# Optimization experiments

Measured on AMD Instinct MI355X. Metric: run time of the kernel, lower is better.

## Reference

```python
import jax, jax.numpy as jnp
import numpy as np

LN_EPS = 1e-5
WKV_EPS = 1e-8
NEG_INF = -1e38


def _layernorm(x, g, b):
    m = jnp.mean(x, axis=-1, keepdims=True)
    v = jnp.mean(jnp.square(x - m), axis=-1, keepdims=True)
    return (x - m) * jax.lax.rsqrt(v + LN_EPS) * g + b


def _wkv(w, u, k, v):
    """RWKV WKV linear recurrence with log-sum-exp stabilized state.
    w,u: (C,); k,v: (B,T,C). Returns y (B,T,C), new_state (B,C,2)."""
    B, T, C = k.shape
    aa0 = jnp.zeros((B, C), k.dtype)
    bb0 = jnp.full((B, C), NEG_INF, k.dtype)

    def step(carry, kv_t):
        aa, bb = carry
        kk, vv = kv_t  # (B,C) each
        ww = u + kk
        p = jnp.maximum(bb, ww)
        e1 = jnp.exp(bb - p)
        e2 = jnp.exp(ww - p)
        y_t = (e1 * aa + e2 * vv) / (e1 + e2 + WKV_EPS)
        ww = w + bb
        p = jnp.maximum(ww, kk)
        e1 = jnp.exp(ww - p)
        e2 = jnp.exp(kk - p)
        aa = e1 * aa + e2 * vv
        bb = p + jnp.log(e1 + e2 + WKV_EPS)
        return (aa, bb), y_t

    (aa, bb), ys = jax.lax.scan(step, (aa0, bb0),
                                (jnp.swapaxes(k, 0, 1), jnp.swapaxes(v, 0, 1)))
    y = jnp.swapaxes(ys, 0, 1)  # (B,T,C)
    new_state = jnp.stack([aa, bb], axis=-1)  # (B,C,2)
    return y, new_state


def setup_inputs() -> dict:
    key = jax.random.key(0)
    ks = jax.random.split(key, 12)
    B, T, C = 8, 2048, 1024
    scale = 0.02
    return {
        "x": jax.random.normal(ks[0], (B, T, C), jnp.float32),
        "time_decay": jax.random.uniform(ks[1], (C,), jnp.float32, -1.0, 1.0),
        "time_first": jax.random.uniform(ks[2], (C,), jnp.float32, -1.0, 1.0),
        "W_tm": jax.random.normal(ks[3], (C, 3 * C), jnp.float32) * scale,
        "g1": jnp.ones((C,), jnp.float32),
        "b1": jnp.zeros((C,), jnp.float32),
        "tmk": jax.random.uniform(ks[4], (1, 1, C), jnp.float32),
        "tmv": jax.random.uniform(ks[5], (1, 1, C), jnp.float32),
        "tmr": jax.random.uniform(ks[6], (1, 1, C), jnp.float32),
        "W_cm": jax.random.normal(ks[7], (C, 4 * C), jnp.float32) * scale,
        "W_cp": jax.random.normal(ks[8], (4 * C, C), jnp.float32) * scale,
        "g2": jnp.ones((C,), jnp.float32),
        "b2": jnp.zeros((C,), jnp.float32),
        "cmk": jax.random.uniform(ks[9], (1, 1, C), jnp.float32),
        "cmr": jax.random.uniform(ks[10], (1, 1, C), jnp.float32),
    }


def reference(x, time_decay, time_first, W_tm, g1, b1, tmk, tmv, tmr,
              W_cm, W_cp, g2, b2, cmk, cmr):
    # ---- time mixing ----
    x_prev = jnp.concatenate([x[:, :1], x[:, :-1]], axis=1)  # shift (state=None)
    kvr = _layernorm(x, g1, b1) @ W_tm  # (B,T,3C)
    k, v, r = jnp.split(kvr, 3, axis=-1)
    k = k * tmk + x_prev * (1.0 - tmk)
    v = v * tmv + x_prev * (1.0 - tmv)
    r = jax.nn.sigmoid(r * tmr + x_prev * (1.0 - tmr))
    y, new_state = _wkv(time_decay, time_first, k, v)
    x = x + r * y
    # ---- channel mixing ----
    xp = jnp.concatenate([x[:, -1:], x[:, :-1]], axis=1)  # as in source
    xn = _layernorm(x, g2, b2)
    kk = xn @ W_cm  # (B,T,4C) hidden
    cmk4 = jnp.tile(cmk, (1, 1, 4))
    xp4 = jnp.tile(xp, (1, 1, 4))
    kk = kk * cmk4 + xp4 * (1.0 - cmk4)
    rr = jax.nn.sigmoid(xn * cmr + xp * (1.0 - cmr))
    vv = jnp.square(jax.nn.relu(kk)) @ W_cp  # (B,T,C)
    x = x + rr * vv
    return x, new_state
```

## Files before the change

kernel.cpp:

```cpp
#include <hip/hip_runtime.h>


#define Bb 8
#define T 2048
#define C 1024
#define M (Bb*T)
#define LCH 32
#define NCH 64
#define NCI (Bb*NCH)
#define WKV_THREADS (NCI*C)

typedef unsigned short u16;
typedef unsigned int u32;
typedef __bf16 bf16x8 __attribute__((ext_vector_type(8)));
typedef float f32x4 __attribute__((ext_vector_type(4)));
typedef u16 u16x4 __attribute__((ext_vector_type(4)));

__device__ __forceinline__ u16 f2bf(float f) {
    u32 u = __float_as_uint(f);
    u32 r = u + 0x7FFFu + ((u >> 16) & 1u);
    return (u16)(r >> 16);
}
__device__ __forceinline__ float bf2f(u16 s) {
    return __uint_as_float(((u32)s) << 16);
}
__device__ __forceinline__ float sigmoidf_(float z) {
    return 1.0f / (1.0f + __expf(-z));
}
__device__ __forceinline__ void load_lds16(const void* g, void* l) {
    __builtin_amdgcn_global_load_lds(
        (const __attribute__((address_space(1))) void*)g,
        (__attribute__((address_space(3))) void*)l, 16, 0, 0);
}

__global__ __launch_bounds__(256) void transpose_cast_kernel(
    const float* __restrict__ W, u16* __restrict__ Wt, int K, int N)
{
    __shared__ float tile[32][33];
    const int bk = blockIdx.x * 32, bn = blockIdx.y * 32;
    const int tx = threadIdx.x, ty = threadIdx.y;
    #pragma unroll
    for (int i = 0; i < 32; i += 8)
        tile[ty + i][tx] = W[(size_t)(bk + ty + i) * N + bn + tx];
    __syncthreads();
    #pragma unroll
    for (int i = 0; i < 32; i += 8)
        Wt[(size_t)(bn + ty + i) * K + bk + tx] = f2bf(tile[tx][ty + i]);
}

__device__ __forceinline__ void gemm_mainloop(
    const u16* __restrict__ A, const int lda,
    const u16* __restrict__ Bt, const int ldb, const int K,
    const int m0, const int n0, u16* Alds, u16* Blds, f32x4 acc[4][4])
{
    const int tid  = threadIdx.x;
    const int wave = tid >> 6, lane = tid & 63;
    const int q = lane >> 4, m16 = lane & 15;
    const int wr = (wave >> 1) << 6, wc = (wave & 1) << 6;

    const f32x4 zero4 = {0.f, 0.f, 0.f, 0.f};
    #pragma unroll
    for (int i = 0; i < 4; i++)
        #pragma unroll
        for (int j = 0; j < 4; j++) acc[i][j] = zero4;

    const int sr = tid >> 3;
    const int sc = (((tid & 7) ^ (sr & 7)) * 8);
    const u16* ag = &A[(size_t)(m0 + sr) * lda + sc];
    const u16* bg = &Bt[(size_t)(n0 + sr) * ldb + sc];
    u16* al = &Alds[tid * 8];
    u16* bl = &Blds[tid * 8];

    const int xh = (m16 & 7);

    for (int k0 = 0; k0 < K; k0 += 64) {
        #pragma unroll
        for (int t = 0; t < 4; ++t) {
            load_lds16(ag + (size_t)(t * 32) * lda + k0, al + t * 2048);
            load_lds16(bg + (size_t)(t * 32) * ldb + k0, bl + t * 2048);
        }
        __syncthreads();
        #pragma unroll
        for (int s = 0; s < 2; ++s) {
            const int ch = ((s * 4 + q) ^ xh) * 8;
            bf16x8 a[4], b[4];
            #pragma unroll
            for (int i = 0; i < 4; i++)
                a[i] = *(const bf16x8*)&Alds[(wr + i * 16 + m16) * 64 + ch];
            #pragma unroll
            for (int j = 0; j < 4; j++)
                b[j] = *(const bf16x8*)&Blds[(wc + j * 16 + m16) * 64 + ch];
            #pragma unroll
            for (int i = 0; i < 4; i++)
                #pragma unroll
                for (int j = 0; j < 4; j++)
                    acc[i][j] = __builtin_amdgcn_mfma_f32_16x16x32_bf16(a[i], b[j], acc[i][j], 0, 0, 0);
        }
        __syncthreads();
    }
}

__global__ __launch_bounds__(256) void ln1_kernel(
    const float* __restrict__ x, const float* __restrict__ g, const float* __restrict__ b,
    u16* __restrict__ xn)
{
    const int row = blockIdx.x, tid = threadIdx.x;
    const size_t base = (size_t)row * C;
    const int c = tid * 4;
    float4 v = *(const float4*)&x[base + c];
    float s  = v.x + v.y + v.z + v.w;
    float s2 = v.x*v.x + v.y*v.y + v.z*v.z + v.w*v.w;
    #pragma unroll
    for (int off = 32; off >= 1; off >>= 1) { s += __shfl_xor(s, off); s2 += __shfl_xor(s2, off); }
    __shared__ float red[8];
    const int wave = tid >> 6, lane = tid & 63;
    if (lane == 0) { red[wave] = s; red[4 + wave] = s2; }
    __syncthreads();
    const float sum  = red[0] + red[1] + red[2] + red[3];
    const float sums = red[4] + red[5] + red[6] + red[7];
    const float mean = sum * (1.0f / C);
    const float var  = sums * (1.0f / C) - mean * mean;
    const float rstd = rsqrtf(var + 1e-5f);
    float4 gv = *(const float4*)&g[c];
    float4 bv = *(const float4*)&b[c];
    u16x4 o;
    o.x = f2bf((v.x - mean) * rstd * gv.x + bv.x);
    o.y = f2bf((v.y - mean) * rstd * gv.y + bv.y);
    o.z = f2bf((v.z - mean) * rstd * gv.z + bv.z);
    o.w = f2bf((v.w - mean) * rstd * gv.w + bv.w);
    *(u16x4*)&xn[base + c] = o;
}

__global__ __launch_bounds__(256) void gemm1_kernel(
    const u16* __restrict__ xn, const u16* __restrict__ wt,
    const float* __restrict__ x,
    const float* __restrict__ tmk, const float* __restrict__ tmv, const float* __restrict__ tmr,
    u16* __restrict__ kvbuf, u16* __restrict__ rbuf)
{
    __shared__ __align__(16) u16 Alds[128 * 64];
    __shared__ __align__(16) u16 Blds[128 * 64];
    f32x4 acc[4][4];
    const int m0 = blockIdx.x * 128, n0 = blockIdx.y * 128;
    gemm_mainloop(xn, C, wt, C, C, m0, n0, Alds, Blds, acc);

    const int tid = threadIdx.x, wave = tid >> 6, lane = tid & 63;
    const int q = lane >> 4, m16 = lane & 15;
    const int wr = (wave >> 1) << 6, wc = (wave & 1) << 6;
    const int grp = n0 >> 10;
    const int cbase = (n0 & 1023) + wc;
    #pragma unroll
    for (int i = 0; i < 4; i++) {
        #pragma unroll
        for (int rg = 0; rg < 4; rg++) {
            const int row = m0 + wr + i * 16 + q * 4 + rg;
            const int t = row & (T - 1);
            const size_t rowp = (size_t)(t ? row - 1 : row) * C;
            #pragma unroll
            for (int j = 0; j < 4; j++) {
                const int cc = cbase + j * 16 + m16;
                const float val = acc[i][j][rg];
                const float xp = x[rowp + cc];
                if (grp == 0) {
                    const float f = tmk[cc];
                    kvbuf[(size_t)row * 2048 + 2 * cc] = f2bf(val * f + xp * (1.0f - f));
                } else if (grp == 1) {
                    const float f = tmv[cc];
                    kvbuf[(size_t)row * 2048 + 2 * cc + 1] = f2bf(val * f + xp * (1.0f - f));
                } else {
                    const float f = tmr[cc];
                    rbuf[(size_t)row * C + cc] = f2bf(sigmoidf_(val * f + xp * (1.0f - f)));
                }
            }
        }
    }
}

__global__ __launch_bounds__(256) void wkv_k1(
    const u32* __restrict__ kvp, const float* __restrict__ wdec, float* __restrict__ bc)
{
    const int tid = blockIdx.x * 256 + threadIdx.x;
    const int c = tid & (C - 1), ci = tid >> 10;
    const float w = wdec[c];
    const size_t L = ((size_t)(ci >> 6) * T + (size_t)(ci & (NCH - 1)) * LCH) * C + c;
    float bb = -1e38f;
    #pragma unroll 4
    for (int t = 0; t < LCH; ++t) {
        const float k = bf2f((u16)(kvp[L + (size_t)t * C] & 0xffffu));
        const float ww = w + bb;
        const float p = fmaxf(ww, k);
        const float e1 = __expf(ww - p), e2 = __expf(k - p);
        bb = p + __logf(e1 + e2 + 1e-8f);
    }
    bc[tid] = bb;
}

__global__ __launch_bounds__(256) void wkv_p1(
    const float* __restrict__ bc, const float* __restrict__ wdec, float* __restrict__ bbin)
{
    const int gid = blockIdx.x * 256 + threadIdx.x;
    const int c = gid & (C - 1), b = gid >> 10;
    const float Lw = (float)LCH * wdec[c];
    float bb = -1e38f;
    #pragma unroll 8
    for (int j = 0; j < NCH; ++j) {
        const int idx = (b * NCH + j) * C + c;
        bbin[idx] = bb;
        const float a = Lw + bb;
        const float bcv = bc[idx];
        const float m = fmaxf(a, bcv);
        bb = m + __logf(__expf(a - m) + __expf(bcv - m));
    }
}

__global__ __launch_bounds__(256) void wkv_k2a(
    const u32* __restrict__ kvp, const float* __restrict__ wdec,
    const float* __restrict__ bbin, float* __restrict__ logS, float* __restrict__ Rr)
{
    const int tid = blockIdx.x * 256 + threadIdx.x;
    const int c = tid & (C - 1), ci = tid >> 10;
    const float w = wdec[c];
    const size_t L = ((size_t)(ci >> 6) * T + (size_t)(ci & (NCH - 1)) * LCH) * C + c;
    float bb = bbin[tid], ls = 0.0f, R = 0.0f;
    #pragma unroll 4
    for (int t = 0; t < LCH; ++t) {
        const u32 kv = kvp[L + (size_t)t * C];
        const float k = bf2f((u16)(kv & 0xffffu)), v = bf2f((u16)(kv >> 16));
        const float ww = w + bb;
        const float p = fmaxf(ww, k);
        const float e1 = __expf(ww - p), e2 = __expf(k - p);
        R = e1 * R + e2 * v;
        ls += ww - p;
        bb = p + __logf(e1 + e2 + 1e-8f);
    }
    logS[tid] = ls;
    Rr[tid] = R;
}

__global__ __launch_bounds__(256) void wkv_p2(
    const float* __restrict__ logS, const float* __restrict__ Rr, float* __restrict__ aain)
{
    const int gid = blockIdx.x * 256 + threadIdx.x;
    const int c = gid & (C - 1), b = gid >> 10;
    float a = 0.0f;
    #pragma unroll 8
    for (int j = 0; j < NCH; ++j) {
        const int idx = (b * NCH + j) * C + c;
        aain[idx] = a;
        a = __expf(logS[idx]) * a + Rr[idx];
    }
}

__global__ __launch_bounds__(256) void wkv_k2c(
    const u32* __restrict__ kvp, const u16* __restrict__ rbuf, const float* __restrict__ x,
    const float* __restrict__ wdec, const float* __restrict__ ufirst,
    const float* __restrict__ bbin, const float* __restrict__ aain,
    float* __restrict__ x2, float* __restrict__ state)
{
    const int tid = blockIdx.x * 256 + threadIdx.x;
    const int c = tid & (C - 1), ci = tid >> 10;
    const int b = ci >> 6, j = ci & (NCH - 1);
    const float w = wdec[c], u = ufirst[c];
    float aa = aain[tid], bb = bbin[tid];
    const size_t L = ((size_t)b * T + (size_t)j * LCH) * C + c;
    #pragma unroll 4
    for (int t = 0; t < LCH; ++t) {
        const size_t idx = L + (size_t)t * C;
        const u32 kv = kvp[idx];
        const float k = bf2f((u16)(kv & 0xffffu)), v = bf2f((u16)(kv >> 16));
        const float r = bf2f(rbuf[idx]), xv = x[idx];
        float ww = u + k;
        float p  = fmaxf(bb, ww);
        float e1 = __expf(bb - p), e2 = __expf(ww - p);
        const float y = (e1 * aa + e2 * v) / (e1 + e2 + 1e-8f);
        x2[idx] = xv + r * y;
        ww = w + bb;
        p  = fmaxf(ww, k);
        e1 = __expf(ww - p); e2 = __expf(k - p);
        aa = e1 * aa + e2 * v;
        bb = p + __logf(e1 + e2 + 1e-8f);
    }
    if (j == NCH - 1) {
        state[2 * (b * C + c)]     = aa;
        state[2 * (b * C + c) + 1] = bb;
    }
}

__global__ __launch_bounds__(256) void ln2_kernel(
    const float* __restrict__ x2, const float* __restrict__ g, const float* __restrict__ b,
    const float* __restrict__ cmr, u16* __restrict__ xn, u16* __restrict__ rr,
    u16* __restrict__ xps)
{
    const int row = blockIdx.x, tid = threadIdx.x;
    const size_t base = (size_t)row * C;
    const int t = row & (T - 1);
    const size_t basep = (size_t)(row - t + (t ? t - 1 : T - 1)) * C;
    const int c = tid * 4;
    float4 v = *(const float4*)&x2[base + c];
    float s  = v.x + v.y + v.z + v.w;
    float s2 = v.x*v.x + v.y*v.y + v.z*v.z + v.w*v.w;
    #pragma unroll
    for (int off = 32; off >= 1; off >>= 1) { s += __shfl_xor(s, off); s2 += __shfl_xor(s2, off); }
    __shared__ float red[8];
    const int wave = tid >> 6, lane = tid & 63;
    if (lane == 0) { red[wave] = s; red[4 + wave] = s2; }
    __syncthreads();
    const float sum  = red[0] + red[1] + red[2] + red[3];
    const float sums = red[4] + red[5] + red[6] + red[7];
    const float mean = sum * (1.0f / C);
    const float var  = sums * (1.0f / C) - mean * mean;
    const float rstd = rsqrtf(var + 1e-5f);
    float4 gv = *(const float4*)&g[c];
    float4 bv = *(const float4*)&b[c];
    float4 fv = *(const float4*)&cmr[c];
    float4 xp = *(const float4*)&x2[basep + c];
    float xn0 = (v.x - mean) * rstd * gv.x + bv.x;
    float xn1 = (v.y - mean) * rstd * gv.y + bv.y;
    float xn2 = (v.z - mean) * rstd * gv.z + bv.z;
    float xn3 = (v.w - mean) * rstd * gv.w + bv.w;
    u16x4 o; o.x = f2bf(xn0); o.y = f2bf(xn1); o.z = f2bf(xn2); o.w = f2bf(xn3);
    *(u16x4*)&xn[base + c] = o;
    u16x4 p4; p4.x = f2bf(xp.x); p4.y = f2bf(xp.y); p4.z = f2bf(xp.z); p4.w = f2bf(xp.w);
    *(u16x4*)&xps[base + c] = p4;
    u16x4 r4;
    r4.x = f2bf(sigmoidf_(xn0 * fv.x + xp.x * (1.0f - fv.x)));
    r4.y = f2bf(sigmoidf_(xn1 * fv.y + xp.y * (1.0f - fv.y)));
    r4.z = f2bf(sigmoidf_(xn2 * fv.z + xp.z * (1.0f - fv.z)));
    r4.w = f2bf(sigmoidf_(xn3 * fv.w + xp.w * (1.0f - fv.w)));
    *(u16x4*)&rr[base + c] = r4;
}

__global__ __launch_bounds__(256) void gemm2_kernel(
    const u16* __restrict__ xn, const u16* __restrict__ wt,
    const u16* __restrict__ xps, const float* __restrict__ cmk,
    u16* __restrict__ hbuf, const int nbase)
{
    __shared__ __align__(16) u16 Alds[128 * 64];
    __shared__ __align__(16) u16 Blds[128 * 64];
    f32x4 acc[4][4];
    const int m0 = blockIdx.x * 128, n0 = blockIdx.y * 128;
    gemm_mainloop(xn, C, wt, C, C, m0, n0, Alds, Blds, acc);

    const int tid = threadIdx.x, wave = tid >> 6, lane = tid & 63;
    const int q = lane >> 4, m16 = lane & 15;
    const int wr = (wave >> 1) << 6, wc = (wave & 1) << 6;
    #pragma unroll
    for (int i = 0; i < 4; i++) {
        #pragma unroll
        for (int rg = 0; rg < 4; rg++) {
            const int row = m0 + wr + i * 16 + q * 4 + rg;
            #pragma unroll
            for (int j = 0; j < 4; j++) {
                const int nloc = n0 + wc + j * 16 + m16;
                const int cc = (nbase + nloc) & (C - 1);
                const float f = cmk[cc];
                const float xp = bf2f(xps[(size_t)row * C + cc]);
                const float kk = acc[i][j][rg] * f + xp * (1.0f - f);
                const float h = fmaxf(kk, 0.0f);
                hbuf[(size_t)row * 2048 + nloc] = f2bf(h * h);
            }
        }
    }
}

__global__ __launch_bounds__(256) void gemm3_kernel(
    const u16* __restrict__ hbuf, const u16* __restrict__ wt,
    const u16* __restrict__ rr, float* __restrict__ out)
{
    __shared__ __align__(16) u16 Alds[128 * 64];
    __shared__ __align__(16) u16 Blds[128 * 64];
    f32x4 acc[4][4];
    const int m0 = blockIdx.x * 128, n0 = blockIdx.y * 128;
    gemm_mainloop(hbuf, 2048, wt, 4096, 2048, m0, n0, Alds, Blds, acc);

    const int tid = threadIdx.x, wave = tid >> 6, lane = tid & 63;
    const int q = lane >> 4, m16 = lane & 15;
    const int wr = (wave >> 1) << 6, wc = (wave & 1) << 6;
    #pragma unroll
    for (int i = 0; i < 4; i++) {
        #pragma unroll
        for (int rg = 0; rg < 4; rg++) {
            const int row = m0 + wr + i * 16 + q * 4 + rg;
            #pragma unroll
            for (int j = 0; j < 4; j++) {
                const int cc = n0 + wc + j * 16 + m16;
                const size_t idx = (size_t)row * C + cc;
                const float base = out[idx];
                out[idx] = base + bf2f(rr[idx]) * acc[i][j][rg];
            }
        }
    }
}

#define OFF_WT_CM  0
#define OFF_WT_CP  8388608
#define OFF_XN     16777216
#define OFF_KV     50331648
#define OFF_H      OFF_KV
#define OFF_RB     117440512
#define OFF_WT_TM  150994944
#define OFF_BC     150994944
#define OFF_BBIN   153092096
#define OFF_LOGS   155189248
#define OFF_RCH    157286400
#define OFF_AAIN   159383552
#define OFF_XPS    150994944

extern "C" void kernel_launch(void* const* d_in, const int* in_sizes, int n_in,
                              void* d_out, int out_size, void* d_ws, size_t ws_size,
                              hipStream_t stream) {
    const float* x          = (const float*)d_in[0];
    const float* time_decay = (const float*)d_in[1];
    const float* time_first = (const float*)d_in[2];
    const float* W_tm       = (const float*)d_in[3];
    const float* g1         = (const float*)d_in[4];
    const float* b1         = (const float*)d_in[5];
    const float* tmk        = (const float*)d_in[6];
    const float* tmv        = (const float*)d_in[7];
    const float* tmr        = (const float*)d_in[8];
    const float* W_cm       = (const float*)d_in[9];
    const float* W_cp       = (const float*)d_in[10];
    const float* g2         = (const float*)d_in[11];
    const float* b2         = (const float*)d_in[12];
    const float* cmk        = (const float*)d_in[13];
    const float* cmr        = (const float*)d_in[14];
    float* out = (float*)d_out;

    char* ws = (char*)d_ws;
    u16*   wt_cm = (u16*)(ws + OFF_WT_CM);
    u16*   wt_cp = (u16*)(ws + OFF_WT_CP);
    u16*   xn    = (u16*)(ws + OFF_XN);
    u16*   kvbuf = (u16*)(ws + OFF_KV);
    u16*   hbuf  = (u16*)(ws + OFF_H);
    u16*   rbuf  = (u16*)(ws + OFF_RB);
    u16*   wt_tm = (u16*)(ws + OFF_WT_TM);
    u16*   xps   = (u16*)(ws + OFF_XPS);
    float* bc    = (float*)(ws + OFF_BC);
    float* bbin  = (float*)(ws + OFF_BBIN);
    float* logS  = (float*)(ws + OFF_LOGS);
    float* Rch   = (float*)(ws + OFF_RCH);
    float* aain  = (float*)(ws + OFF_AAIN);
    float* x2    = out;

    transpose_cast_kernel<<<dim3(1024/32, 3072/32), dim3(32, 8), 0, stream>>>(W_tm, wt_tm, 1024, 3072);
    transpose_cast_kernel<<<dim3(1024/32, 4096/32), dim3(32, 8), 0, stream>>>(W_cm, wt_cm, 1024, 4096);
    transpose_cast_kernel<<<dim3(4096/32, 1024/32), dim3(32, 8), 0, stream>>>(W_cp, wt_cp, 4096, 1024);
    ln1_kernel<<<M, 256, 0, stream>>>(x, g1, b1, xn);
    gemm1_kernel<<<dim3(M/128, 3072/128), 256, 0, stream>>>(xn, wt_tm, x, tmk, tmv, tmr,
                                                            kvbuf, rbuf);
    {
        const u32* kvp = (const u32*)kvbuf;
        wkv_k1 <<<WKV_THREADS/256, 256, 0, stream>>>(kvp, time_decay, bc);
        wkv_p1 <<<(Bb*C)/256, 256, 0, stream>>>(bc, time_decay, bbin);
        wkv_k2a<<<WKV_THREADS/256, 256, 0, stream>>>(kvp, time_decay, bbin, logS, Rch);
        wkv_p2 <<<(Bb*C)/256, 256, 0, stream>>>(logS, Rch, aain);
        wkv_k2c<<<WKV_THREADS/256, 256, 0, stream>>>(kvp, rbuf, x, time_decay, time_first,
                                                     bbin, aain, x2, out + (size_t)M * C);
    }
    ln2_kernel<<<M, 256, 0, stream>>>(x2, g2, b2, cmr, xn, rbuf, xps);
    for (int half = 0; half < 2; ++half) {
        const int nbase = half * 2048;
        gemm2_kernel<<<dim3(M/128, 2048/128), 256, 0, stream>>>(
            xn, wt_cm + (size_t)nbase * C, xps, cmk, hbuf, nbase);
        gemm3_kernel<<<dim3(M/128, 1024/128), 256, 0, stream>>>(
            hbuf, wt_cp + nbase, rbuf, out);
    }
}
```

Measured before the change: 961.2 us.

## Replace 128x128 GEMM mainloop with 256x256 double-buffered 8-wave pipelined mainloop

The three GEMM kernels move from a 128x128 tile with 4 waves and a load-sync-compute loop to a 256x256 tile with 8 waves. The new loop double-buffers LDS across two k-steps and interleaves async global-to-LDS loads with MFMA phases, using manual waitcnt, barriers and setprio. Block IDs are also remapped in groups of 8, which could help cache locality. The intent is to hide memory latency and raise arithmetic intensity per block. In exchange the kernels use far more LDS and registers, have fewer blocks for the smaller GEMMs, and rely on fragile hand-placed waitcnt for correctness. Prefetch indices wrap modulo nkt, so the final iterations issue redundant loads.

Result: faster. 862.9 us (-10.2%).

```diff
diff --git a/kernel.cpp b/kernel.cpp
--- a/kernel.cpp
+++ b/kernel.cpp
@@ -48,56 +48,104 @@
         Wt[(size_t)(bn + ty + i) * K + bk + tx] = f2bf(tile[tx][ty + i]);
 }
 
-__device__ __forceinline__ void gemm_mainloop(
+__device__ __forceinline__ void gemm256_mainloop(
     const u16* __restrict__ A, const int lda,
-    const u16* __restrict__ Bt, const int ldb, const int K,
-    const int m0, const int n0, u16* Alds, u16* Blds, f32x4 acc[4][4])
+    const u16* __restrict__ Bt, const int ldb, const int nkt,
+    const int m0, const int n0, u16* lds, f32x4 acc[2][2][4][2])
 {
     const int tid  = threadIdx.x;
     const int wave = tid >> 6, lane = tid & 63;
     const int q = lane >> 4, m16 = lane & 15;
-    const int wr = (wave >> 1) << 6, wc = (wave & 1) << 6;
+    const int wm = wave >> 2, wn = wave & 3;
 
     const f32x4 zero4 = {0.f, 0.f, 0.f, 0.f};
     #pragma unroll
-    for (int i = 0; i < 4; i++)
-        #pragma unroll
-        for (int j = 0; j < 4; j++) acc[i][j] = zero4;
+    for (int i = 0; i < 2; ++i)
+        #pragma unroll
+        for (int j = 0; j < 2; ++j)
+            #pragma unroll
+            for (int k = 0; k < 4; ++k)
+                #pragma unroll
+                for (int l = 0; l < 2; ++l) acc[i][j][k][l] = zero4;
 
     const int sr = tid >> 3;
-    const int sc = (((tid & 7) ^ (sr & 7)) * 8);
-    const u16* ag = &A[(size_t)(m0 + sr) * lda + sc];
-    const u16* bg = &Bt[(size_t)(n0 + sr) * ldb + sc];
-    u16* al = &Alds[tid * 8];
-    u16* bl = &Blds[tid * 8];
-
-    const int xh = (m16 & 7);
-
-    for (int k0 = 0; k0 < K; k0 += 64) {
-        #pragma unroll
-        for (int t = 0; t < 4; ++t) {
-            load_lds16(ag + (size_t)(t * 32) * lda + k0, al + t * 2048);
-            load_lds16(bg + (size_t)(t * 32) * ldb + k0, bl + t * 2048);
+    const int kc = ((tid & 7) ^ (sr & 7)) << 3;
+    const size_t abase = (size_t)(m0 + sr) * lda + kc;
+    const size_t bbase = (size_t)(n0 + sr) * ldb + kc;
+    const size_t lda64 = (size_t)lda << 6, ldb64 = (size_t)ldb << 6;
+    char* ldsb = (char*)lds;
+    const int dst0 = tid << 4;
+
+#define STG_A(bufs, hf, k0) do { \
+    char* d_ = ldsb + (((bufs) * 4 + (hf)) << 14) + dst0; \
+    const u16* g_ = A + abase + (size_t)(hf) * 2 * lda64 + (k0); \
+    load_lds16(g_, d_); load_lds16(g_ + lda64, d_ + 8192); } while (0)
+#define STG_B(bufs, hf, k0) do { \
+    char* d_ = ldsb + (((bufs) * 4 + 2 + (hf)) << 14) + dst0; \
+    const u16* g_ = Bt + bbase + (size_t)(hf) * 2 * ldb64 + (k0); \
+    load_lds16(g_, d_); load_lds16(g_ + ldb64, d_ + 8192); } while (0)
+
+    STG_A(0, 0, 0);  STG_B(0, 0, 0);  STG_A(0, 1, 0);  STG_B(0, 1, 0);
+    STG_A(1, 0, 64); STG_B(1, 0, 64);
+    asm volatile("s_waitcnt vmcnt(4)" ::: "memory");
+    __builtin_amdgcn_s_barrier();
+
+    const int arow = ((wm << 6) + m16) << 6;
+    const int brow = ((wn << 5) + m16) << 6;
+    const int xh = m16 & 7;
+    const int ch0 = (q ^ xh) << 3, ch1 = ((4 + q) ^ xh) << 3;
+
+    #pragma unroll 1
+    for (int kt2 = 0; kt2 < nkt; kt2 += 2) {
+        #pragma unroll
+        for (int p = 0; p < 8; ++p) {
+            const int pp = p & 3, aa = pp >> 1, bbq = pp & 1, buf = p >> 2;
+            const u16* Ap = lds + ((buf * 4 + aa) << 13) + arow;
+            const u16* Bq = lds + ((buf * 4 + 2 + bbq) << 13) + brow;
+            bf16x8 av[4][2], bv[2][2];
+            #pragma unroll
+            for (int mf = 0; mf < 4; ++mf) {
+                av[mf][0] = *(const bf16x8*)&Ap[mf * 1024 + ch0];
+                av[mf][1] = *(const bf16x8*)&Ap[mf * 1024 + ch1];
+            }
+            #pragma unroll
+            for (int nf = 0; nf < 2; ++nf) {
+                bv[nf][0] = *(const bf16x8*)&Bq[nf * 1024 + ch0];
+                bv[nf][1] = *(const bf16x8*)&Bq[nf * 1024 + ch1];
+            }
+            {
+                const int k1 = ((kt2 + 1) & (nkt - 1)) << 6;
+                const int k2 = ((kt2 + 2) & (nkt - 1)) << 6;
+                const int k3 = ((kt2 + 3) & (nkt - 1)) << 6;
+                if (p == 0)      STG_A(1, 1, k1);
+                else if (p == 1) STG_B(1, 1, k1);
+                else if (p == 2) STG_A(0, 0, k2);
+                else if (p == 3) STG_B(0, 0, k2);
+                else if (p == 4) STG_A(0, 1, k2);
+                else if (p == 5) STG_B(0, 1, k2);
+                else if (p == 6) STG_A(1, 0, k3);
+                else             STG_B(1, 0, k3);
+            }
+            __builtin_amdgcn_s_barrier();
+            asm volatile("s_waitcnt lgkmcnt(0)" ::: "memory");
+            __builtin_amdgcn_s_setprio(1);
+            #pragma unroll
+            for (int mf = 0; mf < 4; ++mf)
+                #pragma unroll
+                for (int nf = 0; nf < 2; ++nf) {
+                    acc[aa][bbq][mf][nf] = __builtin_amdgcn_mfma_f32_16x16x32_bf16(
+                        av[mf][0], bv[nf][0], acc[aa][bbq][mf][nf], 0, 0, 0);
+                    acc[aa][bbq][mf][nf] = __builtin_amdgcn_mfma_f32_16x16x32_bf16(
+                        av[mf][1], bv[nf][1], acc[aa][bbq][mf][nf], 0, 0, 0);
+                }
+            __builtin_amdgcn_s_setprio(0);
+            if (pp == 3) asm volatile("s_waitcnt vmcnt(4)" ::: "memory");
+            __builtin_amdgcn_s_barrier();
         }
-        __syncthreads();
-        #pragma unroll
-        for (int s = 0; s < 2; ++s) {
-            const int ch = ((s * 4 + q) ^ xh) * 8;
-            bf16x8 a[4], b[4];
-            #pragma unroll
-            for (int i = 0; i < 4; i++)
-                a[i] = *(const bf16x8*)&Alds[(wr + i * 16 + m16) * 64 + ch];
-            #pragma unroll
-            for (int j = 0; j < 4; j++)
-                b[j] = *(const bf16x8*)&Blds[(wc + j * 16 + m16) * 64 + ch];
-            #pragma unroll
-            for (int i = 0; i < 4; i++)
-                #pragma unroll
-                for (int j = 0; j < 4; j++)
-                    acc[i][j] = __builtin_amdgcn_mfma_f32_16x16x32_bf16(a[i], b[j], acc[i][j], 0, 0, 0);
-        }
-        __syncthreads();
-    }
+    }
+    asm volatile("s_waitcnt vmcnt(0)" ::: "memory");
+#undef STG_A
+#undef STG_B
 }
 
 __global__ __launch_bounds__(256) void ln1_kernel(
@@ -131,45 +179,49 @@
     *(u16x4*)&xn[base + c] = o;
 }
 
-__global__ __launch_bounds__(256) void gemm1_kernel(
+__global__ __launch_bounds__(512, 2) void gemm1_kernel(
     const u16* __restrict__ xn, const u16* __restrict__ wt,
     const float* __restrict__ x,
     const float* __restrict__ tmk, const float* __restrict__ tmv, const float* __restrict__ tmr,
     u16* __restrict__ kvbuf, u16* __restrict__ rbuf)
 {
-    __shared__ __align__(16) u16 Alds[128 * 64];
-    __shared__ __align__(16) u16 Blds[128 * 64];
-    f32x4 acc[4][4];
-    const int m0 = blockIdx.x * 128, n0 = blockIdx.y * 128;
-    gemm_mainloop(xn, C, wt, C, C, m0, n0, Alds, Blds, acc);
+    __shared__ __align__(16) u16 lds[8 * 8192];
+    f32x4 acc[2][2][4][2];
+    const int nbn = 12;
+    int id = blockIdx.x;
+    id = (id & 7) * (768 >> 3) + (id >> 3);
+    const int m0 = (id / nbn) << 8, n0 = (id % nbn) << 8;
+    gemm256_mainloop(xn, C, wt, C, 16, m0, n0, lds, acc);
 
     const int tid = threadIdx.x, wave = tid >> 6, lane = tid & 63;
     const int q = lane >> 4, m16 = lane & 15;
-    const int wr = (wave >> 1) << 6, wc = (wave & 1) << 6;
+    const int wm = wave >> 2, wn = wave & 3;
     const int grp = n0 >> 10;
-    const int cbase = (n0 & 1023) + wc;
-    #pragma unroll
-    for (int i = 0; i < 4; i++) {
-        #pragma unroll
-        for (int rg = 0; rg < 4; rg++) {
-            const int row = m0 + wr + i * 16 + q * 4 + rg;
-            const int t = row & (T - 1);
-            const size_t rowp = (size_t)(t ? row - 1 : row) * C;
-            #pragma unroll
-            for (int j = 0; j < 4; j++) {
-                const int cc = cbase + j * 16 + m16;
-                const float val = acc[i][j][rg];
-                const float xp = x[rowp + cc];
-                if (grp == 0) {
-                    const float f = tmk[cc];
-                    kvbuf[(size_t)row * 2048 + 2 * cc] = f2bf(val * f + xp * (1.0f - f));
-                } else if (grp == 1) {
-                    const float f = tmv[cc];
-                    kvbuf[(size_t)row * 2048 + 2 * cc + 1] = f2bf(val * f + xp * (1.0f - f));
-                } else {
-                    const float f = tmr[cc];
-                    rbuf[(size_t)row * C + cc] = f2bf(sigmoidf_(val * f + xp * (1.0f - f)));
-                }
+    #pragma unroll
+    for (int a2 = 0; a2 < 2; ++a2)
+    #pragma unroll
+    for (int mf = 0; mf < 4; ++mf)
+    #pragma unroll
+    for (int rg = 0; rg < 4; ++rg) {
+        const int row = m0 + a2 * 128 + wm * 64 + mf * 16 + q * 4 + rg;
+        const int t = row & (T - 1);
+        const size_t rowp = (size_t)(t ? row - 1 : row) * C;
+        #pragma unroll
+        for (int b2 = 0; b2 < 2; ++b2)
+        #pragma unroll
+        for (int nf = 0; nf < 2; ++nf) {
+            const int cc = (n0 + b2 * 128 + wn * 32 + nf * 16 + m16) & (C - 1);
+            const float val = acc[a2][b2][mf][nf][rg];
+            const float xp = x[rowp + cc];
+            if (grp == 0) {
+                const float f = tmk[cc];
+                kvbuf[(size_t)row * 2048 + 2 * cc] = f2bf(val * f + xp * (1.0f - f));
+            } else if (grp == 1) {
+                const float f = tmv[cc];
+                kvbuf[(size_t)row * 2048 + 2 * cc + 1] = f2bf(val * f + xp * (1.0f - f));
+            } else {
+                const float f = tmr[cc];
+                rbuf[(size_t)row * C + cc] = f2bf(sigmoidf_(val * f + xp * (1.0f - f)));
             }
         }
     }
@@ -329,64 +381,74 @@
     *(u16x4*)&rr[base + c] = r4;
 }
 
-__global__ __launch_bounds__(256) void gemm2_kernel(
+__global__ __launch_bounds__(512, 2) void gemm2_kernel(
     const u16* __restrict__ xn, const u16* __restrict__ wt,
     const u16* __restrict__ xps, const float* __restrict__ cmk,
     u16* __restrict__ hbuf, const int nbase)
 {
-    __shared__ __align__(16) u16 Alds[128 * 64];
-    __shared__ __align__(16) u16 Blds[128 * 64];
-    f32x4 acc[4][4];
-    const int m0 = blockIdx.x * 128, n0 = blockIdx.y * 128;
-    gemm_mainloop(xn, C, wt, C, C, m0, n0, Alds, Blds, acc);
+    __shared__ __align__(16) u16 lds[8 * 8192];
+    f32x4 acc[2][2][4][2];
+    const int nbn = 8;
+    int id = blockIdx.x;
+    id = (id & 7) * (512 >> 3) + (id >> 3);
+    const int m0 = (id / nbn) << 8, n0 = (id % nbn) << 8;
+    gemm256_mainloop(xn, C, wt, C, 16, m0, n0, lds, acc);
 
     const int tid = threadIdx.x, wave = tid >> 6, lane = tid & 63;
     const int q = lane >> 4, m16 = lane & 15;
-    const int wr = (wave >> 1) << 6, wc = (wave & 1) << 6;
-    #pragma unroll
-    for (int i = 0; i < 4; i++) {
-        #pragma unroll
-        for (int rg = 0; rg < 4; rg++) {
-            const int row = m0 + wr + i * 16 + q * 4 + rg;
-            #pragma unroll
-            for (int j = 0; j < 4; j++) {
-                const int nloc = n0 + wc + j * 16 + m16;
-                const int cc = (nbase + nloc) & (C - 1);
-                const float f = cmk[cc];
-                const float xp = bf2f(xps[(size_t)row * C + cc]);
-                const float kk = acc[i][j][rg] * f + xp * (1.0f - f);
-                const float h = fmaxf(kk, 0.0f);
-                hbuf[(size_t)row * 2048 + nloc] = f2bf(h * h);
-            }
+    const int wm = wave >> 2, wn = wave & 3;
+    #pragma unroll
+    for (int a2 = 0; a2 < 2; ++a2)
+    #pragma unroll
+    for (int mf = 0; mf < 4; ++mf)
+    #pragma unroll
+    for (int rg = 0; rg < 4; ++rg) {
+        const int row = m0 + a2 * 128 + wm * 64 + mf * 16 + q * 4 + rg;
+        #pragma unroll
+        for (int b2 = 0; b2 < 2; ++b2)
+        #pragma unroll
+        for (int nf = 0; nf < 2; ++nf) {
+            const int nloc = n0 + b2 * 128 + wn * 32 + nf * 16 + m16;
+            const int cc = (nbase + nloc) & (C - 1);
+            const float f = cmk[cc];
+            const float xp = bf2f(xps[(size_t)row * C + cc]);
+            const float kk = acc[a2][b2][mf][nf][rg] * f + xp * (1.0f - f);
+            const float h = fmaxf(kk, 0.0f);
+            hbuf[(size_t)row * 2048 + nloc] = f2bf(h * h);
         }
     }
 }
 
-__global__ __launch_bounds__(256) void gemm3_kernel(
+__global__ __launch_bounds__(512, 2) void gemm3_kernel(
     const u16* __restrict__ hbuf, const u16* __restrict__ wt,
     const u16* __restrict__ rr, float* __restrict__ out)
 {
-    __shared__ __align__(16) u16 Alds[128 * 64];
-    __shared__ __align__(16) u16 Blds[128 * 64];
-    f32x4 acc[4][4];
-    const int m0 = blockIdx.x * 128, n0 = blockIdx.y * 128;
-    gemm_mainloop(hbuf, 2048, wt, 4096, 2048, m0, n0, Alds, Blds, acc);
+    __shared__ __align__(16) u16 lds[8 * 8192];
+    f32x4 acc[2][2][4][2];
+    const int nbn = 4;
+    int id = blockIdx.x;
+    id = (id & 7) * (256 >> 3) + (id >> 3);
+    const int m0 = (id / nbn) << 8, n0 = (id % nbn) << 8;
+    gemm256_mainloop(hbuf, 2048, wt, 4096, 32, m0, n0, lds, acc);
 
     const int tid = threadIdx.x, wave = tid >> 6, lane = tid & 63;
     const int q = lane >> 4, m16 = lane & 15;
-    const int wr = (wave >> 1) << 6, wc = (wave & 1) << 6;
-    #pragma unroll
-    for (int i = 0; i < 4; i++) {
-        #pragma unroll
-        for (int rg = 0; rg < 4; rg++) {
-            const int row = m0 + wr + i * 16 + q * 4 + rg;
-            #pragma unroll
-            for (int j = 0; j < 4; j++) {
-                const int cc = n0 + wc + j * 16 + m16;
-                const size_t idx = (size_t)row * C + cc;
-                const float base = out[idx];
-                out[idx] = base + bf2f(rr[idx]) * acc[i][j][rg];
-            }
+    const int wm = wave >> 2, wn = wave & 3;
+    #pragma unroll
+    for (int a2 = 0; a2 < 2; ++a2)
+    #pragma unroll
+    for (int mf = 0; mf < 4; ++mf)
+    #pragma unroll
+    for (int rg = 0; rg < 4; ++rg) {
+        const int row = m0 + a2 * 128 + wm * 64 + mf * 16 + q * 4 + rg;
+        #pragma unroll
+        for (int b2 = 0; b2 < 2; ++b2)
+        #pragma unroll
+        for (int nf = 0; nf < 2; ++nf) {
+            const int cc = n0 + b2 * 128 + wn * 32 + nf * 16 + m16;
+            const size_t idx = (size_t)row * C + cc;
+            const float base = out[idx];
+            out[idx] = base + bf2f(rr[idx]) * acc[a2][b2][mf][nf][rg];
         }
     }
 }
@@ -445,8 +507,7 @@
     transpose_cast_kernel<<<dim3(1024/32, 4096/32), dim3(32, 8), 0, stream>>>(W_cm, wt_cm, 1024, 4096);
     transpose_cast_kernel<<<dim3(4096/32, 1024/32), dim3(32, 8), 0, stream>>>(W_cp, wt_cp, 4096, 1024);
     ln1_kernel<<<M, 256, 0, stream>>>(x, g1, b1, xn);
-    gemm1_kernel<<<dim3(M/128, 3072/128), 256, 0, stream>>>(xn, wt_tm, x, tmk, tmv, tmr,
-                                                            kvbuf, rbuf);
+    gemm1_kernel<<<768, 512, 0, stream>>>(xn, wt_tm, x, tmk, tmv, tmr, kvbuf, rbuf);
     {
         const u32* kvp = (const u32*)kvbuf;
         wkv_k1 <<<WKV_THREADS/256, 256, 0, stream>>>(kvp, time_decay, bc);
@@ -459,9 +520,9 @@
     ln2_kernel<<<M, 256, 0, stream>>>(x2, g2, b2, cmr, xn, rbuf, xps);
     for (int half = 0; half < 2; ++half) {
         const int nbase = half * 2048;
-        gemm2_kernel<<<dim3(M/128, 2048/128), 256, 0, stream>>>(
+        gemm2_kernel<<<512, 512, 0, stream>>>(
             xn, wt_cm + (size_t)nbase * C, xps, cmk, hbuf, nbase);
-        gemm3_kernel<<<dim3(M/128, 1024/128), 256, 0, stream>>>(
+        gemm3_kernel<<<256, 512, 0, stream>>>(
             hbuf, wt_cp + nbase, rbuf, out);
     }
 }
```
